# Kernel optimization log

Hardware: AMD Instinct MI355X
Metric: run time of the kernel (lower is better)

## Reference

```python
import jax, jax.numpy as jnp
import numpy as np

V = 32000   # vocab
E = 512     # hidden_size (d_model)
NH = 8      # num_heads
DH = E // NH
NL = 2      # num_layers
FF = 2048   # TransformerDecoderLayer default dim_feedforward
MAXLEN = 24 # cfg.max_length -> gen_len (no target given)
S, B = 48, 8
TRANS = 14
INIT = TRANS - 2            # tgt = transform[1:-1]
LF = INIT + MAXLEN - 1      # final tgt length after the loop
EPS = 1e-5
NEG = -1e9


def pos_encoding(length, d):
    pos = np.arange(length, dtype=np.float32)[:, None]
    div = np.exp(-np.log(10000.0) * np.arange(0, d, 2, dtype=np.float32) / d)
    pe = np.zeros((length, d), dtype=np.float32)
    pe[:, 0::2] = np.sin(pos * div)
    pe[:, 1::2] = np.cos(pos * div)
    return jnp.asarray(pe)


def setup_inputs() -> dict:
    key = jax.random.key(0)
    ks = jax.random.split(key, 12)
    s = 0.02
    return {
        "enc_outputs": jax.random.normal(ks[0], (S, B, E), jnp.float32),
        "transform": jax.random.randint(ks[1], (TRANS, B), 0, V),
        "tf_ratio": 0,
        "emb_table": jax.random.normal(ks[2], (V, E), jnp.float32) * s,
        "sa_w": jax.random.normal(ks[3], (NL, 3 * E, E), jnp.float32) * s,
        "sa_b": jnp.zeros((NL, 3 * E), jnp.float32),
        "sa_ow": jax.random.normal(ks[4], (NL, E, E), jnp.float32) * s,
        "sa_ob": jnp.zeros((NL, E), jnp.float32),
        "ca_w": jax.random.normal(ks[5], (NL, 3 * E, E), jnp.float32) * s,
        "ca_b": jnp.zeros((NL, 3 * E), jnp.float32),
        "ca_ow": jax.random.normal(ks[6], (NL, E, E), jnp.float32) * s,
        "ca_ob": jnp.zeros((NL, E), jnp.float32),
        "ff1_w": jax.random.normal(ks[7], (NL, FF, E), jnp.float32) * s,
        "ff1_b": jnp.zeros((NL, FF), jnp.float32),
        "ff2_w": jax.random.normal(ks[8], (NL, E, FF), jnp.float32) * s,
        "ff2_b": jnp.zeros((NL, E), jnp.float32),
        "ln_g": jnp.ones((NL, 3, E), jnp.float32),
        "ln_b": jnp.zeros((NL, 3, E), jnp.float32),
        "out_w": jax.random.normal(ks[9], (V, E), jnp.float32) * s,
        "out_b": jnp.zeros((V,), jnp.float32),
    }


def _ln(x, g, b):
    m = jnp.mean(x, -1, keepdims=True)
    v = jnp.mean((x - m) ** 2, -1, keepdims=True)
    return (x - m) * jax.lax.rsqrt(v + EPS) * g + b


def _mha(q_in, kv_in, w, b, ow, ob, mask):
    # q_in [Lq,B,E], kv_in [Lk,B,E]; PyTorch packed in_proj [3E,E]
    wq, wk, wv = jnp.split(w, 3, 0)
    bq, bk, bv = jnp.split(b, 3, 0)
    proj = lambda x, wm, bm: (x @ wm.T + bm).reshape(x.shape[0], x.shape[1], NH, DH)
    q, k, v = proj(q_in, wq, bq), proj(kv_in, wk, bk), proj(kv_in, wv, bv)
    sc = jnp.einsum('qbhd,kbhd->bhqk', q, k) / np.sqrt(DH).astype(np.float32)
    if mask is not None:
        sc = sc + mask
    a = jax.nn.softmax(sc, -1)
    o = jnp.einsum('bhqk,kbhd->qbhd', a, v).reshape(q_in.shape[0], q_in.shape[1], E)
    return o @ ow.T + ob


def _decoder(x, mem, mask, p):
    # post-norm TransformerDecoderLayer: self-attn -> cross-attn -> relu FFN
    for l in range(NL):
        x = _ln(x + _mha(x, x, p['sa_w'][l], p['sa_b'][l], p['sa_ow'][l], p['sa_ob'][l], mask),
                p['ln_g'][l, 0], p['ln_b'][l, 0])
        x = _ln(x + _mha(x, mem, p['ca_w'][l], p['ca_b'][l], p['ca_ow'][l], p['ca_ob'][l], None),
                p['ln_g'][l, 1], p['ln_b'][l, 1])
        h = jax.nn.relu(x @ p['ff1_w'][l].T + p['ff1_b'][l]) @ p['ff2_w'][l].T + p['ff2_b'][l]
        x = _ln(x + h, p['ln_g'][l, 2], p['ln_b'][l, 2])
    return x


def reference(enc_outputs, transform, tf_ratio, emb_table, sa_w, sa_b, sa_ow, sa_ob,
              ca_w, ca_b, ca_ow, ca_ob, ff1_w, ff1_b, ff2_w, ff2_b, ln_g, ln_b,
              out_w, out_b):
    # tf_ratio == 0 -> no teacher forcing; gen_len = max_length (no target attr)
    p = dict(sa_w=sa_w, sa_b=sa_b, sa_ow=sa_ow, sa_ob=sa_ob, ca_w=ca_w, ca_b=ca_b,
             ca_ow=ca_ow, ca_ob=ca_ob, ff1_w=ff1_w, ff1_b=ff1_b, ff2_w=ff2_w,
             ff2_b=ff2_b, ln_g=ln_g, ln_b=ln_b)
    pe = pos_encoding(MAXLEN, E)
    # causal mask over the fixed-size buffer; padded (future) slots cannot
    # influence valid positions, so full-buffer passes == torch prefix passes.
    mask = jnp.where(jnp.tril(jnp.ones((LF, LF), bool)), 0.0, NEG)
    tgt0 = emb_table[transform[1:-1]] + pe[:INIT][:, None, :]   # [INIT,B,E]
    buf = jnp.zeros((LF, B, E), jnp.float32).at[:INIT].set(tgt0)

    def step(buf, i):
        h = _decoder(buf, enc_outputs, mask, p)
        pos = INIT - 1 + i                        # last valid position
        pred = jnp.argmax(h[pos] @ out_w.T + out_b, axis=-1)   # [B]
        # torch re-embeds the single predicted token -> PE position 0
        emb = emb_table[pred] + pe[0]
        return buf.at[pos + 1].set(emb), None

    buf, _ = jax.lax.scan(step, buf, jnp.arange(MAXLEN - 1))
    h = _decoder(buf, enc_outputs, mask, p)       # final loop iteration's pass
    return h @ out_w.T + out_b                    # dec_outputs [LF,B,V]
```

## Files before the change

### kernel.cpp

```cpp
#include <hip/hip_runtime.h>
#include <hip/hip_bf16.h>
#include <math.h>

#define V    32000
#define E    512
#define NH   8
#define DH   64
#define NL   2
#define FF   2048
#define MAXLEN 24
#define S    48
#define B    8
#define TRANS 14
#define INIT 12
#define LF   35

#define NB   256
#define NT   512

typedef float f4 __attribute__((ext_vector_type(4)));

__device__ inline float wsum(float v) {
#pragma unroll
  for (int off = 32; off; off >>= 1) v += __shfl_xor(v, off);
  return v;
}
__device__ inline float wmax(float v) {
#pragma unroll
  for (int off = 32; off; off >>= 1) v = fmaxf(v, __shfl_xor(v, off));
  return v;
}

__device__ inline float ldc(const float* p) {
  return __hip_atomic_load(p, __ATOMIC_RELAXED, __HIP_MEMORY_SCOPE_AGENT);
}
__device__ inline void stc(float* p, float v) {
  __hip_atomic_store(p, v, __ATOMIC_RELAXED, __HIP_MEMORY_SCOPE_AGENT);
}
__device__ inline float2 ldc8(const float* p) {
  union { unsigned long long u; float2 f; } c;
  c.u = __hip_atomic_load((const unsigned long long*)p, __ATOMIC_RELAXED, __HIP_MEMORY_SCOPE_AGENT);
  return c.f;
}
__device__ inline void stc8(float* p, float x, float y) {
  union { unsigned long long u; float f[2]; } c; c.f[0] = x; c.f[1] = y;
  __hip_atomic_store((unsigned long long*)p, c.u, __ATOMIC_RELAXED, __HIP_MEMORY_SCOPE_AGENT);
}
__device__ inline int ldci(const int* p) {
  return __hip_atomic_load(p, __ATOMIC_RELAXED, __HIP_MEMORY_SCOPE_AGENT);
}

__device__ inline void ld8_bypass(const float* p, f4* w) {
  asm volatile(
      "global_load_dwordx4 %0, %8, off sc0 sc1 nt\n\t"
      "global_load_dwordx4 %1, %8, off offset:16 sc0 sc1 nt\n\t"
      "global_load_dwordx4 %2, %8, off offset:32 sc0 sc1 nt\n\t"
      "global_load_dwordx4 %3, %8, off offset:48 sc0 sc1 nt\n\t"
      "global_load_dwordx4 %4, %8, off offset:64 sc0 sc1 nt\n\t"
      "global_load_dwordx4 %5, %8, off offset:80 sc0 sc1 nt\n\t"
      "global_load_dwordx4 %6, %8, off offset:96 sc0 sc1 nt\n\t"
      "global_load_dwordx4 %7, %8, off offset:112 sc0 sc1 nt\n\t"
      "s_waitcnt vmcnt(0)"
      : "=&v"(w[0]), "=&v"(w[1]), "=&v"(w[2]), "=&v"(w[3]),
        "=&v"(w[4]), "=&v"(w[5]), "=&v"(w[6]), "=&v"(w[7])
      : "v"(p));
}

#define CMB(v, idx, ov, oi) do { if ((ov) > (v) || ((ov) == (v) && (oi) < (idx))) { (v) = (ov); (idx) = (oi); } } while (0)


__global__ void embed_init_k(const int* __restrict__ transform, const float* __restrict__ emb,
                             float* __restrict__ xbuf) {
  int t = blockIdx.x;
  int pos = t >> 3, b = t & 7;
  int tok = transform[(1 + pos) * B + b];
  for (int d = threadIdx.x; d < E; d += blockDim.x) {
    double div = exp(-log(10000.0) * (double)(d & ~1) / (double)E);
    double ang = (double)pos * div;
    float pe = (d & 1) ? (float)cos(ang) : (float)sin(ang);
    xbuf[(size_t)t * E + d] = emb[(size_t)tok * E + d] + pe;
  }
}

template <int K>
__global__ __launch_bounds__(256) void gemm_k(
    const float* __restrict__ x, const float* __restrict__ W, const float* __restrict__ bias,
    int ntok, int nout, int route, int relu,
    float* __restrict__ out0, float* __restrict__ out1, float* __restrict__ out2) {
  constexpr int K4 = K / 4;
  constexpr int J  = K / 256;
  __shared__ float4 xt[8][K4];
  const int tid = threadIdx.x;
  const int lane = tid & 63;
  const int o = blockIdx.x * 4 + (tid >> 6);

  float4 wr[J];
  if (o < nout) {
    const float4* Wr = (const float4*)(W + (size_t)o * K);
#pragma unroll
    for (int j = 0; j < J; ++j) wr[j] = Wr[lane + 64 * j];
  }

  const int ng = ntok >> 3;
  for (int g = 0; g < ng; ++g) {
    if (g) __syncthreads();
    const float4* xg = (const float4*)(x + (size_t)g * 8 * K);
    float4* xf = &xt[0][0];
    for (int i = tid; i < 8 * K4; i += 256) xf[i] = xg[i];
    __syncthreads();
    if (o < nout) {
      float acc[8] = {0, 0, 0, 0, 0, 0, 0, 0};
#pragma unroll
      for (int j = 0; j < J; ++j) {
        float4 w = wr[j];
#pragma unroll
        for (int tt = 0; tt < 8; ++tt) {
          float4 xv = xt[tt][lane + 64 * j];
          acc[tt] += w.x * xv.x + w.y * xv.y + w.z * xv.z + w.w * xv.w;
        }
      }
#pragma unroll
      for (int tt = 0; tt < 8; ++tt) acc[tt] = wsum(acc[tt]);
      if (lane == 0) {
        float bo = bias[o];
#pragma unroll
        for (int tt = 0; tt < 8; ++tt) {
          float v = acc[tt] + bo;
          if (relu) v = fmaxf(v, 0.f);
          int t = g * 8 + tt;
          if (route == 0) {
            out0[(size_t)t * nout + o] = v;
          } else if (route == 1) {
            if (o < E) out0[(size_t)t * E + o] = v;
            else if (o < 2 * E) out1[(size_t)t * E + (o - E)] = v;
            else out2[(size_t)t * E + (o - 2 * E)] = v;
          } else {
            if (o < E) out0[(size_t)t * E + o] = v;
            else out1[(size_t)t * E + (o - E)] = v;
          }
        }
      }
    }
  }
}

__global__ __launch_bounds__(256) void attn_k(
    const float* __restrict__ q, const float* __restrict__ Kc, const float* __restrict__ Vc,
    float* __restrict__ outp, int p0, int nq, int nk_fixed, int causal) {
  const int tid = threadIdx.x;
  const int lane = tid & 63;
  const int u = blockIdx.x * 4 + (tid >> 6);
  if (u >= nq * 64) return;
  const int qi = u >> 6;
  const int r = u & 63;
  const int b = r >> 3, h = r & 7;
  const int nk = causal ? (p0 + qi + 1) : nk_fixed;

  const size_t qoff = (size_t)(qi * B + b) * E + h * DH + lane;
  const float qv = q[qoff];

  float myscore = -INFINITY;
  for (int k = 0; k < nk; ++k) {
    float prod = qv * Kc[(size_t)(k * B + b) * E + h * DH + lane];
    prod = wsum(prod);
    if (lane == k) myscore = prod * 0.125f;
  }
  float m = wmax(myscore);
  float p = (lane < nk) ? expf(myscore - m) : 0.f;
  float denom = wsum(p);
  float a = p / denom;

  float oacc = 0.f;
  for (int k = 0; k < nk; ++k) {
    float ak = __shfl(a, k);
    oacc = fmaf(ak, Vc[(size_t)(k * B + b) * E + h * DH + lane], oacc);
  }
  outp[qoff] = oacc;
}

__global__ __launch_bounds__(256) void add_ln_k(
    const float* __restrict__ xa, const float* __restrict__ xb,
    const float* __restrict__ g, const float* __restrict__ beta,
    float* __restrict__ outp, int ntok) {
  const int tid = threadIdx.x, lane = tid & 63;
  const int t = blockIdx.x * 4 + (tid >> 6);
  if (t >= ntok) return;
  float v[8];
  float s = 0.f;
#pragma unroll
  for (int j = 0; j < 8; ++j) {
    int d = lane + 64 * j;
    v[j] = xa[(size_t)t * E + d] + xb[(size_t)t * E + d];
    s += v[j];
  }
  s = wsum(s);
  float mean = s * (1.f / 512.f);
  float d2 = 0.f;
#pragma unroll
  for (int j = 0; j < 8; ++j) { float dd = v[j] - mean; d2 += dd * dd; }
  d2 = wsum(d2);
  float inv = 1.f / sqrtf(d2 * (1.f / 512.f) + 1e-5f);
#pragma unroll
  for (int j = 0; j < 8; ++j) {
    int d = lane + 64 * j;
    outp[(size_t)t * E + d] = (v[j] - mean) * inv * g[d] + beta[d];
  }
}

#define B_QKV 0
#define B_OW  6144
#define B_CQ  8192
#define B_COW 10240
#define B_FF1 12288
#define B_FF2 20480
#define SW_TOT 28672

__global__ __launch_bounds__(NT, 1) void decode_persist_k(
    const float* __restrict__ emb,
    const float* __restrict__ sa_w, const float* __restrict__ sa_b,
    const float* __restrict__ sa_ow, const float* __restrict__ sa_ob,
    const float* __restrict__ ca_w, const float* __restrict__ ca_b,
    const float* __restrict__ ca_ow, const float* __restrict__ ca_ob,
    const float* __restrict__ ff1_w, const float* __restrict__ ff1_b,
    const float* __restrict__ ff2_w, const float* __restrict__ ff2_b,
    const float* __restrict__ ln_g, const float* __restrict__ ln_b,
    const float* __restrict__ out_w, const float* __restrict__ out_b,
    float* __restrict__ kself, float* __restrict__ vself,
    const float* __restrict__ kcross, const float* __restrict__ vcross,
    float* __restrict__ xstep, float* __restrict__ qbuf, float* __restrict__ attbuf,
    float* __restrict__ rawbuf, float* __restrict__ x1buf, float* __restrict__ x2buf,
    float* __restrict__ x3buf, float* __restrict__ ybuf, float* __restrict__ hbuf,
    float* __restrict__ pbuf, float* __restrict__ amaxbuf,
    float* __restrict__ outp, int* __restrict__ bar) {
  __shared__ __align__(16) float s_w[SW_TOT];
  __shared__ __align__(16) float s_x[8 * E];
  __shared__ __align__(16) float s_y[8 * E];
  __shared__ __align__(16) float s_q2[64];
  __shared__ float s_rv[NT];
  __shared__ int   s_ri[NT];
  __shared__ float s_pv[8][8];
  __shared__ int   s_pi[8][8];

  const int tid  = threadIdx.x;
  const int lane = tid & 63;
  const int wv   = tid >> 6;
  const int g4   = lane >> 2;
  const int s4   = lane & 3;
  const int bid  = blockIdx.x;
  int gen = 0;

  auto gbar = [&]() {
    ++gen;
    __syncthreads();
    if (tid == 0)
      __hip_atomic_fetch_add(&bar[(bid & 31) * 32], 1, __ATOMIC_RELAXED, __HIP_MEMORY_SCOPE_AGENT);
    if (wv == 0) {
      const int target = gen * 8;
      for (;;) {
        int c = ldci(&bar[(lane & 31) * 32]);
        if (__all(c >= target)) break;
        __builtin_amdgcn_s_sleep(2);
      }
    }
    __syncthreads();
  };

  auto stage_in = [&](float* dst, const float* src) {
    for (int k = tid; k < 2048; k += NT) {
      float2 vv = ldc8(src + 2 * k);
      dst[2 * k] = vv.x; dst[2 * k + 1] = vv.y;
    }
  };
  auto lnstage = [&](int lnidx) {
    const float* gg = ln_g + (size_t)lnidx * E;
    const float* be = ln_b + (size_t)lnidx * E;
    float v[8]; float sum = 0.f;
#pragma unroll
    for (int j = 0; j < 8; ++j) {
      int d = lane + 64 * j;
      v[j] = s_x[wv * E + d] + s_y[wv * E + d];
      sum += v[j];
    }
    sum = wsum(sum);
    float mean = sum * (1.f / 512.f);
    float d2 = 0.f;
#pragma unroll
    for (int j = 0; j < 8; ++j) { float dd = v[j] - mean; d2 += dd * dd; }
    d2 = wsum(d2);
    float inv = 1.f / sqrtf(d2 * (1.f / 512.f) + 1e-5f);
#pragma unroll
    for (int j = 0; j < 8; ++j) {
      int d = lane + 64 * j;
      s_x[wv * E + d] = (v[j] - mean) * inv * gg[d] + be[d];
    }
    __syncthreads();
  };
  auto publish = [&](float* dst) {
    for (int k = tid; k < 256; k += NT)
      stc8(&dst[bid * E + 2 * k], s_x[bid * E + 2 * k], s_x[bid * E + 2 * k + 1]);
  };
  auto proj2 = [&](int wbase, const float* biasp, float* dst) {
    const int row = wv & 1;
    const int r = bid * 2 + row;
    const f4* wp = (const f4*)&s_w[wbase + row * 512];
    f4 w0 = wp[lane], w1 = wp[lane + 64];
    float bias = biasp[r];
#pragma unroll
    for (int half = 0; half < 2; ++half) {
      int b = (wv >> 1) + half * 4;
      const f4* x4 = (const f4*)&s_x[b * E];
      f4 a = w0 * x4[lane] + w1 * x4[lane + 64];
      float acc = a.x + a.y + a.z + a.w;
      acc = wsum(acc);
      if (lane == 0) stc(&dst[b * E + r], acc + bias);
    }
  };
  auto attn_stage = [&](const float* Kbase, const float* Vbase, int nk) {
    const int b = bid >> 3, h = bid & 7;
    if (wv == 0) {
      s_q2[lane] = ldc(&qbuf[b * E + h * DH + lane]);
      float sc = -INFINITY;
      if (lane < nk) {
        const f4* Kr = (const f4*)(Kbase + ((size_t)lane * B + b) * E + h * DH);
        const f4* Qp = (const f4*)s_q2;
        float a0 = 0.f;
#pragma unroll
        for (int u = 0; u < 16; ++u) {
          f4 kv = Kr[u], qv = Qp[u];
          a0 += kv.x * qv.x + kv.y * qv.y + kv.z * qv.z + kv.w * qv.w;
        }
        sc = a0 * 0.125f;
      }
      float m = wmax(sc);
      float e = (lane < nk) ? expf(sc - m) : 0.f;
      float den = wsum(e);
      float aa = e / den;
      float oa = 0.f;
#pragma unroll 4
      for (int k2 = 0; k2 < nk; ++k2) {
        float ak = __shfl(aa, k2);
        oa = fmaf(ak, Vbase[((size_t)k2 * B + b) * E + h * DH + lane], oa);
      }
      stc(&attbuf[b * E + h * DH + lane], oa);
    }
  };

  {
    auto cprow = [&](const float* src, int dstf) {
      f4* d = (f4*)&s_w[dstf];
      const f4* s = (const f4*)src;
      for (int k = tid; k < 128; k += NT) d[k] = s[k];
    };
    const int kc = bid >> 6;
    for (int l = 0; l < NL; ++l) {
      for (int j = 0; j < 6; ++j)
        cprow(sa_w + ((size_t)l * 1536 + bid * 6 + j) * E, B_QKV + (l * 6 + j) * 512);
      for (int j = 0; j < 2; ++j) {
        cprow(sa_ow + ((size_t)l * 512 + bid * 2 + j) * E, B_OW + (l * 2 + j) * 512);
        cprow(ca_w + ((size_t)l * 1536 + bid * 2 + j) * E, B_CQ + (l * 2 + j) * 512);
        cprow(ca_ow + ((size_t)l * 512 + bid * 2 + j) * E, B_COW + (l * 2 + j) * 512);
      }
      for (int j = 0; j < 8; ++j) {
        cprow(ff1_w + ((size_t)l * FF + bid * 8 + j) * E, B_FF1 + (l * 8 + j) * 512);
        cprow(ff2_w + ((size_t)l * 512 + (bid & 63) * 8 + j) * FF + kc * 512,
              B_FF2 + (l * 8 + j) * 512);
      }
    }
    __syncthreads();
  }

  for (int i = 0; i < MAXLEN - 1; ++i) {
    const int p = INIT + i;

    if (bid < 8) {
      const int b = bid;
      if (i == 0) {
        const float* row = outp + ((size_t)(INIT - 1) * B + b) * V;
        float bv = -INFINITY; int bi = 0x7fffffff;
        for (int j2 = tid; j2 < V / 2; j2 += NT) {
          float2 vv = ldc8(row + 2 * j2);
          CMB(bv, bi, vv.x, 2 * j2);
          CMB(bv, bi, vv.y, 2 * j2 + 1);
        }
        s_rv[tid] = bv; s_ri[tid] = bi;
      } else {
        if (tid < 256) {
          float2 pr = ldc8(&amaxbuf[(size_t)(tid * 8 + b) * 2]);
          s_rv[tid] = pr.x; s_ri[tid] = (int)pr.y;
        } else { s_rv[tid] = -INFINITY; s_ri[tid] = 0x7fffffff; }
      }
      __syncthreads();
      for (int st2 = NT / 2; st2; st2 >>= 1) {
        if (tid < st2) {
          float ov = s_rv[tid + st2]; int oi = s_ri[tid + st2];
          CMB(s_rv[tid], s_ri[tid], ov, oi);
        }
        __syncthreads();
      }
      const int tok = s_ri[0];
      if (tid < 256) {
        int d0 = tid * 2;
        float e0 = emb[(size_t)tok * E + d0];
        float e1 = emb[(size_t)tok * E + d0 + 1] + 1.0f;
        stc8(&xstep[(size_t)b * E + d0], e0, e1);
      }
    }
    gbar();

    for (int l = 0; l < NL; ++l) {
      if (l == 0) {
        stage_in(s_x, xstep);
        __syncthreads();
      } else {
        stage_in(s_x, x2buf); stage_in(s_y, ybuf);
        __syncthreads();
        lnstage(2);
        if (bid < 8) publish(x3buf);
      }
      if (wv < 6) {
        const int r = bid * 6 + wv;
        const int sec = r >> 9, off = r & 511;
        const f4* wp = (const f4*)&s_w[B_QKV + (l * 6 + wv) * 512];
        f4 w0 = wp[lane], w1 = wp[lane + 64];
        float bias = sa_b[(size_t)l * 1536 + r];
#pragma unroll
        for (int b = 0; b < 8; ++b) {
          const f4* x4 = (const f4*)&s_x[b * E];
          f4 a = w0 * x4[lane] + w1 * x4[lane + 64];
          float acc = a.x + a.y + a.z + a.w;
          acc = wsum(acc);
          if (lane == 0) {
            acc += bias;
            if (sec == 0) stc(&qbuf[b * E + off], acc);
            else if (sec == 1) stc(&kself[((size_t)(l * LF + p) * B + b) * E + off], acc);
            else stc(&vself[((size_t)(l * LF + p) * B + b) * E + off], acc);
          }
        }
      }
      gbar();
      if (bid < 64) attn_stage(kself + (size_t)l * LF * B * E, vself + (size_t)l * LF * B * E, p + 1);
      gbar();
      stage_in(s_x, attbuf);
      __syncthreads();
      proj2(B_OW + l * 1024, sa_ob + (size_t)l * 512, rawbuf);
      gbar();
      stage_in(s_x, (l == 0) ? xstep : x3buf); stage_in(s_y, rawbuf);
      __syncthreads();
      lnstage(l * 3 + 0);
      if (bid < 8) publish(x1buf);
      proj2(B_CQ + l * 1024, ca_b + (size_t)l * 1536, qbuf);
      gbar();
      if (bid < 64) attn_stage(kcross + (size_t)l * S * B * E, vcross + (size_t)l * S * B * E, S);
      gbar();
      stage_in(s_x, attbuf);
      __syncthreads();
      proj2(B_COW + l * 1024, ca_ob + (size_t)l * 512, rawbuf);
      gbar();
      stage_in(s_x, x1buf); stage_in(s_y, rawbuf);
      __syncthreads();
      lnstage(l * 3 + 1);
      if (bid < 8) publish(x2buf);
      {
        const int r = bid * 8 + wv;
        const f4* wp = (const f4*)&s_w[B_FF1 + (l * 8 + wv) * 512];
        f4 w0 = wp[lane], w1 = wp[lane + 64];
        float bias = ff1_b[(size_t)l * FF + r];
#pragma unroll
        for (int b = 0; b < 8; ++b) {
          const f4* x4 = (const f4*)&s_x[b * E];
          f4 a = w0 * x4[lane] + w1 * x4[lane + 64];
          float acc = a.x + a.y + a.z + a.w;
          acc = wsum(acc);
          if (lane == 0) stc(&hbuf[b * FF + r], fmaxf(acc + bias, 0.f));
        }
      }
      gbar();
      {
        const int kc = bid >> 6;
        for (int k = tid; k < 2048; k += NT) {
          int b = k >> 8, d2 = (k & 255) * 2;
          float2 vv = ldc8(&hbuf[b * FF + kc * 512 + d2]);
          s_x[b * E + d2] = vv.x; s_x[b * E + d2 + 1] = vv.y;
        }
        __syncthreads();
        const int rowf = (bid & 63) * 8 + wv;
        const f4* wp = (const f4*)&s_w[B_FF2 + (l * 8 + wv) * 512];
        f4 w0 = wp[lane], w1 = wp[lane + 64];
#pragma unroll
        for (int b = 0; b < 8; ++b) {
          const f4* x4 = (const f4*)&s_x[b * E];
          f4 a = w0 * x4[lane] + w1 * x4[lane + 64];
          float acc = a.x + a.y + a.z + a.w;
          acc = wsum(acc);
          if (lane == 0) stc(&pbuf[(size_t)(kc * 512 + rowf) * 8 + b], acc);
        }
      }
      gbar();
      {
        const int row = bid * 2 + (wv & 1);
#pragma unroll
        for (int half = 0; half < 2; ++half) {
          int b = (wv >> 1) + half * 4;
          if (lane == 0) {
            float y = ff2_b[(size_t)l * 512 + row];
#pragma unroll
            for (int kc = 0; kc < 4; ++kc) y += ldc(&pbuf[(size_t)(kc * 512 + row) * 8 + b]);
            stc(&ybuf[b * E + row], y);
          }
        }
      }
      gbar();
    }

    stage_in(s_x, x2buf); stage_in(s_y, ybuf);
    __syncthreads();
    lnstage(5);
    {
      const int idx = wv * 16 + g4;
      const bool valid = idx < 125;
      const int r = bid * 125 + idx;
      float acc[8] = {0, 0, 0, 0, 0, 0, 0, 0};
      if (valid) {
        const float* wrow = out_w + (size_t)r * E + s4 * 128;
#pragma unroll
        for (int seg = 0; seg < 4; ++seg) {
          f4 w8[8];
          ld8_bypass(wrow + seg * 32, w8);
#pragma unroll
          for (int b = 0; b < 8; ++b) {
            const f4* x4 = (const f4*)&s_x[b * E + s4 * 128 + seg * 32];
#pragma unroll
            for (int q = 0; q < 8; ++q) {
              f4 xx = x4[q];
              acc[b] += w8[q].x * xx.x + w8[q].y * xx.y + w8[q].z * xx.z + w8[q].w * xx.w;
            }
          }
        }
#pragma unroll
        for (int b = 0; b < 8; ++b) {
          acc[b] += __shfl_xor(acc[b], 1);
          acc[b] += __shfl_xor(acc[b], 2);
          acc[b] += out_b[r];
        }
        if (s4 == 0) {
#pragma unroll
          for (int b = 0; b < 8; ++b)
            stc(&outp[((size_t)p * B + b) * V + r], acc[b]);
        }
      }
#pragma unroll
      for (int b = 0; b < 8; ++b) {
        float v = valid ? acc[b] : -INFINITY;
        int ix = valid ? r : 0x7fffffff;
#pragma unroll
        for (int off = 1; off < 64; off <<= 1) {
          float ov = __shfl_xor(v, off); int oi = __shfl_xor(ix, off);
          CMB(v, ix, ov, oi);
        }
        if (lane == 0) { s_pv[wv][b] = v; s_pi[wv][b] = ix; }
      }
      __syncthreads();
      if (wv == 0) {
        int b = lane & 7, w2 = lane >> 3;
        float v = s_pv[w2][b]; int ix = s_pi[w2][b];
#pragma unroll
        for (int off = 8; off < 64; off <<= 1) {
          float ov = __shfl_xor(v, off); int oi = __shfl_xor(ix, off);
          CMB(v, ix, ov, oi);
        }
        if (lane < 8) stc8(&amaxbuf[(size_t)(bid * 8 + lane) * 2], v, (float)ix);
      }
    }
    gbar();
  }
}

extern "C" void kernel_launch(void* const* d_in, const int* in_sizes, int n_in,
                              void* d_out, int out_size, void* d_ws, size_t ws_size,
                              hipStream_t stream) {
  const float* enc       = (const float*)d_in[0];
  const int*   transform = (const int*)d_in[1];
  const float* emb       = (const float*)d_in[3];
  const float* sa_w  = (const float*)d_in[4];
  const float* sa_b  = (const float*)d_in[5];
  const float* sa_ow = (const float*)d_in[6];
  const float* sa_ob = (const float*)d_in[7];
  const float* ca_w  = (const float*)d_in[8];
  const float* ca_b  = (const float*)d_in[9];
  const float* ca_ow = (const float*)d_in[10];
  const float* ca_ob = (const float*)d_in[11];
  const float* ff1_w = (const float*)d_in[12];
  const float* ff1_b = (const float*)d_in[13];
  const float* ff2_w = (const float*)d_in[14];
  const float* ff2_b = (const float*)d_in[15];
  const float* ln_g  = (const float*)d_in[16];
  const float* ln_b  = (const float*)d_in[17];
  const float* out_w = (const float*)d_in[18];
  const float* out_b = (const float*)d_in[19];
  float* out = (float*)d_out;

  const size_t SELF_SZ  = (size_t)LF * B * E;
  const size_t CROSS_SZ = (size_t)S * B * E;
  float* ws     = (float*)d_ws;
  float* xbuf   = ws;
  float* kself  = xbuf + (size_t)INIT * B * E;
  float* vself  = kself + NL * SELF_SZ;
  float* kcross = vself + NL * SELF_SZ;
  float* vcross = kcross + NL * CROSS_SZ;
  float* xstep  = vcross + NL * CROSS_SZ;
  float* qbuf   = xstep + 8 * E;
  float* attbuf = qbuf + 8 * E;
  float* rawbuf = attbuf + 8 * E;
  float* x1buf  = rawbuf + 8 * E;
  float* x2buf  = x1buf + 8 * E;
  float* x3buf  = x2buf + 8 * E;
  float* ybuf   = x3buf + 8 * E;
  float* hbuf   = ybuf + 8 * E;
  float* pbuf   = hbuf + 8 * FF;
  float* amaxb  = pbuf + 4 * 512 * 8;
  int*   bar    = (int*)(amaxb + 256 * 8 * 2);
  float* act1   = (float*)(bar + 1024);
  float* act2   = act1 + 96 * E;
  float* act3   = act2 + 96 * E;
  float* ffb    = act3 + 96 * E;

  hipMemsetAsync(bar, 0, 4096, stream);

  embed_init_k<<<INIT * B, 128, 0, stream>>>(transform, emb, xbuf);

  for (int l = 0; l < NL; ++l) {
    gemm_k<E><<<(2 * E) / 4, 256, 0, stream>>>(
        enc, ca_w + ((size_t)l * 3 * E + E) * E, ca_b + (size_t)l * 3 * E + E,
        S * B, 2 * E, 2, 0, kcross + l * CROSS_SZ, vcross + l * CROSS_SZ, nullptr);
  }

  {
    const int p0 = 0, nq = INIT, ntok = nq * B;
    const float* xin = xbuf;
    for (int l = 0; l < NL; ++l) {
      const float* x = (l == 0) ? xin : act1;
      gemm_k<E><<<(3 * E) / 4, 256, 0, stream>>>(
          x, sa_w + (size_t)l * 3 * E * E, sa_b + (size_t)l * 3 * E, ntok, 3 * E, 1, 0,
          act2, kself + l * SELF_SZ, vself + l * SELF_SZ);
      attn_k<<<nq * 16, 256, 0, stream>>>(act2, kself + l * SELF_SZ, vself + l * SELF_SZ,
                                          act3, p0, nq, 0, 1);
      gemm_k<E><<<E / 4, 256, 0, stream>>>(
          act3, sa_ow + (size_t)l * E * E, sa_ob + (size_t)l * E, ntok, E, 0, 0, act2, nullptr, nullptr);
      add_ln_k<<<(ntok + 3) / 4, 256, 0, stream>>>(
          x, act2, ln_g + (size_t)l * 3 * E, ln_b + (size_t)l * 3 * E, act1, ntok);
      gemm_k<E><<<E / 4, 256, 0, stream>>>(
          act1, ca_w + (size_t)l * 3 * E * E, ca_b + (size_t)l * 3 * E, ntok, E, 0, 0, act2, nullptr, nullptr);
      attn_k<<<nq * 16, 256, 0, stream>>>(act2, kcross + l * CROSS_SZ, vcross + l * CROSS_SZ,
                                          act3, p0, nq, S, 0);
      gemm_k<E><<<E / 4, 256, 0, stream>>>(
          act3, ca_ow + (size_t)l * E * E, ca_ob + (size_t)l * E, ntok, E, 0, 0, act2, nullptr, nullptr);
      add_ln_k<<<(ntok + 3) / 4, 256, 0, stream>>>(
          act1, act2, ln_g + (size_t)l * 3 * E + E, ln_b + (size_t)l * 3 * E + E, act1, ntok);
      gemm_k<E><<<FF / 4, 256, 0, stream>>>(
          act1, ff1_w + (size_t)l * FF * E, ff1_b + (size_t)l * FF, ntok, FF, 0, 1, ffb, nullptr, nullptr);
      gemm_k<FF><<<E / 4, 256, 0, stream>>>(
          ffb, ff2_w + (size_t)l * E * FF, ff2_b + (size_t)l * E, ntok, E, 0, 0, act2, nullptr, nullptr);
      add_ln_k<<<(ntok + 3) / 4, 256, 0, stream>>>(
          act1, act2, ln_g + (size_t)l * 3 * E + 2 * E, ln_b + (size_t)l * 3 * E + 2 * E, act1, ntok);
    }
    gemm_k<E><<<V / 4, 256, 0, stream>>>(
        act1, out_w, out_b, ntok, V, 0, 0, out, nullptr, nullptr);
  }

  decode_persist_k<<<NB, NT, 0, stream>>>(
      emb, sa_w, sa_b, sa_ow, sa_ob, ca_w, ca_b, ca_ow, ca_ob,
      ff1_w, ff1_b, ff2_w, ff2_b, ln_g, ln_b, out_w, out_b,
      kself, vself, kcross, vcross,
      xstep, qbuf, attbuf, rawbuf, x1buf, x2buf, x3buf, ybuf, hbuf, pbuf, amaxb,
      out, bar);
}
```

Baseline: 5.523 ms.

## Restructure persistent decode kernel: redundant per-block state, fewer grid barriers, 1024 threads

Doubles the block size of the persistent decode kernel. Every block now keeps its own copy of the residual stream and LayerNorm results in LDS, so the separate publish and stage steps are gone. Each block also computes the argmax and embedding itself, which removes a grid barrier at the start of each step. FF2 is rewritten to cover the full K dimension per block, split across layers by block half, which drops the partial-sum buffer and its extra barrier. The grid barrier changes from atomic counters to per-block flag stores, and the output projection switches from nontemporal asm loads to plain vector loads. In exchange, the same work is repeated across all blocks, and each barrier now polls 256 flags.

```diff
diff --git a/kernel.cpp b/kernel.cpp
--- a/kernel.cpp
+++ b/kernel.cpp
@@ -16,7 +16,7 @@
 #define LF   35
 
 #define NB   256
-#define NT   512
+#define NT   1024
 
 typedef float f4 __attribute__((ext_vector_type(4)));
 
@@ -49,21 +49,8 @@
 __device__ inline int ldci(const int* p) {
   return __hip_atomic_load(p, __ATOMIC_RELAXED, __HIP_MEMORY_SCOPE_AGENT);
 }
-
-__device__ inline void ld8_bypass(const float* p, f4* w) {
-  asm volatile(
-      "global_load_dwordx4 %0, %8, off sc0 sc1 nt\n\t"
-      "global_load_dwordx4 %1, %8, off offset:16 sc0 sc1 nt\n\t"
-      "global_load_dwordx4 %2, %8, off offset:32 sc0 sc1 nt\n\t"
-      "global_load_dwordx4 %3, %8, off offset:48 sc0 sc1 nt\n\t"
-      "global_load_dwordx4 %4, %8, off offset:64 sc0 sc1 nt\n\t"
-      "global_load_dwordx4 %5, %8, off offset:80 sc0 sc1 nt\n\t"
-      "global_load_dwordx4 %6, %8, off offset:96 sc0 sc1 nt\n\t"
-      "global_load_dwordx4 %7, %8, off offset:112 sc0 sc1 nt\n\t"
-      "s_waitcnt vmcnt(0)"
-      : "=&v"(w[0]), "=&v"(w[1]), "=&v"(w[2]), "=&v"(w[3]),
-        "=&v"(w[4]), "=&v"(w[5]), "=&v"(w[6]), "=&v"(w[7])
-      : "v"(p));
+__device__ inline void stci(int* p, int v) {
+  __hip_atomic_store(p, v, __ATOMIC_RELAXED, __HIP_MEMORY_SCOPE_AGENT);
 }
 
 #define CMB(v, idx, ov, oi) do { if ((ov) > (v) || ((ov) == (v) && (oi) < (idx))) { (v) = (ov); (idx) = (oi); } } while (0)
@@ -227,93 +214,85 @@
     const float* __restrict__ out_w, const float* __restrict__ out_b,
     float* __restrict__ kself, float* __restrict__ vself,
     const float* __restrict__ kcross, const float* __restrict__ vcross,
-    float* __restrict__ xstep, float* __restrict__ qbuf, float* __restrict__ attbuf,
-    float* __restrict__ rawbuf, float* __restrict__ x1buf, float* __restrict__ x2buf,
-    float* __restrict__ x3buf, float* __restrict__ ybuf, float* __restrict__ hbuf,
-    float* __restrict__ pbuf, float* __restrict__ amaxbuf,
+    float* __restrict__ qbuf, float* __restrict__ attbuf, float* __restrict__ rawbuf,
+    float* __restrict__ hbuf, float* __restrict__ amaxbuf,
     float* __restrict__ outp, int* __restrict__ bar) {
   __shared__ __align__(16) float s_w[SW_TOT];
   __shared__ __align__(16) float s_x[8 * E];
-  __shared__ __align__(16) float s_y[8 * E];
+  __shared__ __align__(16) float s_raw[8 * E];
   __shared__ __align__(16) float s_q2[64];
-  __shared__ float s_rv[NT];
-  __shared__ int   s_ri[NT];
-  __shared__ float s_pv[8][8];
-  __shared__ int   s_pi[8][8];
+  __shared__ __align__(16) float s_attw[64];
+  __shared__ __align__(16) float s_part[4][64];
+  __shared__ int   s_tok[8];
+  __shared__ float s_pv[16][8];
+  __shared__ int   s_pi[16][8];
 
   const int tid  = threadIdx.x;
   const int lane = tid & 63;
   const int wv   = tid >> 6;
-  const int g4   = lane >> 2;
-  const int s4   = lane & 3;
   const int bid  = blockIdx.x;
   int gen = 0;
 
   auto gbar = [&]() {
     ++gen;
     __syncthreads();
-    if (tid == 0)
-      __hip_atomic_fetch_add(&bar[(bid & 31) * 32], 1, __ATOMIC_RELAXED, __HIP_MEMORY_SCOPE_AGENT);
+    if (tid == 0) stci(&bar[bid * 32], gen);
     if (wv == 0) {
-      const int target = gen * 8;
       for (;;) {
-        int c = ldci(&bar[(lane & 31) * 32]);
-        if (__all(c >= target)) break;
-        __builtin_amdgcn_s_sleep(2);
+        int c0 = ldci(&bar[lane * 32]);
+        int c1 = ldci(&bar[(lane + 64) * 32]);
+        int c2 = ldci(&bar[(lane + 128) * 32]);
+        int c3 = ldci(&bar[(lane + 192) * 32]);
+        if (__all(c0 >= gen && c1 >= gen && c2 >= gen && c3 >= gen)) break;
+        __builtin_amdgcn_s_sleep(1);
       }
     }
     __syncthreads();
   };
 
-  auto stage_in = [&](float* dst, const float* src) {
+  auto stage_raw = [&](const float* src) {
     for (int k = tid; k < 2048; k += NT) {
       float2 vv = ldc8(src + 2 * k);
-      dst[2 * k] = vv.x; dst[2 * k + 1] = vv.y;
-    }
+      s_raw[2 * k] = vv.x; s_raw[2 * k + 1] = vv.y;
+    }
+    __syncthreads();
   };
   auto lnstage = [&](int lnidx) {
-    const float* gg = ln_g + (size_t)lnidx * E;
-    const float* be = ln_b + (size_t)lnidx * E;
-    float v[8]; float sum = 0.f;
-#pragma unroll
-    for (int j = 0; j < 8; ++j) {
-      int d = lane + 64 * j;
-      v[j] = s_x[wv * E + d] + s_y[wv * E + d];
-      sum += v[j];
-    }
-    sum = wsum(sum);
-    float mean = sum * (1.f / 512.f);
-    float d2 = 0.f;
-#pragma unroll
-    for (int j = 0; j < 8; ++j) { float dd = v[j] - mean; d2 += dd * dd; }
-    d2 = wsum(d2);
-    float inv = 1.f / sqrtf(d2 * (1.f / 512.f) + 1e-5f);
-#pragma unroll
-    for (int j = 0; j < 8; ++j) {
-      int d = lane + 64 * j;
-      s_x[wv * E + d] = (v[j] - mean) * inv * gg[d] + be[d];
+    if (wv < 8) {
+      const float* gg = ln_g + (size_t)lnidx * E;
+      const float* be = ln_b + (size_t)lnidx * E;
+      float v[8]; float sum = 0.f;
+#pragma unroll
+      for (int j = 0; j < 8; ++j) {
+        int d = lane + 64 * j;
+        v[j] = s_x[wv * E + d] + s_raw[wv * E + d];
+        sum += v[j];
+      }
+      sum = wsum(sum);
+      float mean = sum * (1.f / 512.f);
+      float d2 = 0.f;
+#pragma unroll
+      for (int j = 0; j < 8; ++j) { float dd = v[j] - mean; d2 += dd * dd; }
+      d2 = wsum(d2);
+      float inv = 1.f / sqrtf(d2 * (1.f / 512.f) + 1e-5f);
+#pragma unroll
+      for (int j = 0; j < 8; ++j) {
+        int d = lane + 64 * j;
+        s_x[wv * E + d] = (v[j] - mean) * inv * gg[d] + be[d];
+      }
     }
     __syncthreads();
   };
-  auto publish = [&](float* dst) {
-    for (int k = tid; k < 256; k += NT)
-      stc8(&dst[bid * E + 2 * k], s_x[bid * E + 2 * k], s_x[bid * E + 2 * k + 1]);
-  };
-  auto proj2 = [&](int wbase, const float* biasp, float* dst) {
-    const int row = wv & 1;
-    const int r = bid * 2 + row;
-    const f4* wp = (const f4*)&s_w[wbase + row * 512];
+  auto proj16 = [&](int wbase, const float* srcLDS, const float* biasp, float* dst) {
+    int j = wv & 1, b = wv >> 1;
+    int r = bid * 2 + j;
+    const f4* wp = (const f4*)&s_w[wbase + j * 512];
     f4 w0 = wp[lane], w1 = wp[lane + 64];
-    float bias = biasp[r];
-#pragma unroll
-    for (int half = 0; half < 2; ++half) {
-      int b = (wv >> 1) + half * 4;
-      const f4* x4 = (const f4*)&s_x[b * E];
-      f4 a = w0 * x4[lane] + w1 * x4[lane + 64];
-      float acc = a.x + a.y + a.z + a.w;
-      acc = wsum(acc);
-      if (lane == 0) stc(&dst[b * E + r], acc + bias);
-    }
+    const f4* x4 = (const f4*)(srcLDS + b * E);
+    f4 a = w0 * x4[lane] + w1 * x4[lane + 64];
+    float acc = a.x + a.y + a.z + a.w;
+    acc = wsum(acc);
+    if (lane == 0) stc(&dst[b * E + r], acc + biasp[r]);
   };
   auto attn_stage = [&](const float* Kbase, const float* Vbase, int nk) {
     const int b = bid >> 3, h = bid & 7;
@@ -326,32 +305,34 @@
         float a0 = 0.f;
 #pragma unroll
         for (int u = 0; u < 16; ++u) {
-          f4 kv = Kr[u], qv = Qp[u];
-          a0 += kv.x * qv.x + kv.y * qv.y + kv.z * qv.z + kv.w * qv.w;
+          f4 kv = Kr[u], qq = Qp[u];
+          a0 += kv.x * qq.x + kv.y * qq.y + kv.z * qq.z + kv.w * qq.w;
         }
         sc = a0 * 0.125f;
       }
       float m = wmax(sc);
       float e = (lane < nk) ? expf(sc - m) : 0.f;
       float den = wsum(e);
-      float aa = e / den;
-      float oa = 0.f;
-#pragma unroll 4
-      for (int k2 = 0; k2 < nk; ++k2) {
-        float ak = __shfl(aa, k2);
-        oa = fmaf(ak, Vbase[((size_t)k2 * B + b) * E + h * DH + lane], oa);
-      }
-      stc(&attbuf[b * E + h * DH + lane], oa);
-    }
+      s_attw[lane] = e / den;
+    }
+    __syncthreads();
+    if (wv < 4) {
+      float o = 0.f;
+      for (int k = wv; k < nk; k += 4)
+        o = fmaf(s_attw[k], Vbase[((size_t)k * B + b) * E + h * DH + lane], o);
+      s_part[wv][lane] = o;
+    }
+    __syncthreads();
+    if (wv == 0)
+      stc(&attbuf[b * E + h * DH + lane],
+          s_part[0][lane] + s_part[1][lane] + s_part[2][lane] + s_part[3][lane]);
   };
 
   {
     auto cprow = [&](const float* src, int dstf) {
-      f4* d = (f4*)&s_w[dstf];
-      const f4* s = (const f4*)src;
+      f4* d = (f4*)&s_w[dstf]; const f4* s = (const f4*)src;
       for (int k = tid; k < 128; k += NT) d[k] = s[k];
     };
-    const int kc = bid >> 6;
     for (int l = 0; l < NL; ++l) {
       for (int j = 0; j < 6; ++j)
         cprow(sa_w + ((size_t)l * 1536 + bid * 6 + j) * E, B_QKV + (l * 6 + j) * 512);
@@ -360,11 +341,14 @@
         cprow(ca_w + ((size_t)l * 1536 + bid * 2 + j) * E, B_CQ + (l * 2 + j) * 512);
         cprow(ca_ow + ((size_t)l * 512 + bid * 2 + j) * E, B_COW + (l * 2 + j) * 512);
       }
-      for (int j = 0; j < 8; ++j) {
+      for (int j = 0; j < 8; ++j)
         cprow(ff1_w + ((size_t)l * FF + bid * 8 + j) * E, B_FF1 + (l * 8 + j) * 512);
-        cprow(ff2_w + ((size_t)l * 512 + (bid & 63) * 8 + j) * FF + kc * 512,
-              B_FF2 + (l * 8 + j) * 512);
-      }
+    }
+    const int lf2 = bid >> 7;
+    for (int j = 0; j < 4; ++j) {
+      f4* d = (f4*)&s_w[B_FF2 + j * 2048];
+      const f4* s = (const f4*)(ff2_w + ((size_t)lf2 * 512 + (bid & 127) * 4 + j) * FF);
+      for (int k = tid; k < 512; k += NT) d[k] = s[k];
     }
     __syncthreads();
   }
@@ -372,59 +356,49 @@
   for (int i = 0; i < MAXLEN - 1; ++i) {
     const int p = INIT + i;
 
-    if (bid < 8) {
-      const int b = bid;
+    {
+      int bw = wv & 7;
+      float v = -INFINITY; int ix = 0x7fffffff;
       if (i == 0) {
-        const float* row = outp + ((size_t)(INIT - 1) * B + b) * V;
-        float bv = -INFINITY; int bi = 0x7fffffff;
-        for (int j2 = tid; j2 < V / 2; j2 += NT) {
-          float2 vv = ldc8(row + 2 * j2);
-          CMB(bv, bi, vv.x, 2 * j2);
-          CMB(bv, bi, vv.y, 2 * j2 + 1);
-        }
-        s_rv[tid] = bv; s_ri[tid] = bi;
+        const float* row = outp + ((size_t)(INIT - 1) * B + bw) * V;
+        for (int jj = lane; jj < V / 2; jj += 64) {
+          float2 t = ldc8(row + 2 * jj);
+          CMB(v, ix, t.x, 2 * jj);
+          CMB(v, ix, t.y, 2 * jj + 1);
+        }
       } else {
-        if (tid < 256) {
-          float2 pr = ldc8(&amaxbuf[(size_t)(tid * 8 + b) * 2]);
-          s_rv[tid] = pr.x; s_ri[tid] = (int)pr.y;
-        } else { s_rv[tid] = -INFINITY; s_ri[tid] = 0x7fffffff; }
-      }
+#pragma unroll
+        for (int t = 0; t < 4; ++t) {
+          int e = lane * 4 + t;
+          float2 pr = ldc8(&amaxbuf[(size_t)(e * 8 + bw) * 2]);
+          CMB(v, ix, pr.x, (int)pr.y);
+        }
+      }
+#pragma unroll
+      for (int off = 1; off < 64; off <<= 1) {
+        float ov = __shfl_xor(v, off); int oi = __shfl_xor(ix, off);
+        CMB(v, ix, ov, oi);
+      }
+      if (lane == 0 && wv < 8) s_tok[bw] = ix;
       __syncthreads();
-      for (int st2 = NT / 2; st2; st2 >>= 1) {
-        if (tid < st2) {
-          float ov = s_rv[tid + st2]; int oi = s_ri[tid + st2];
-          CMB(s_rv[tid], s_ri[tid], ov, oi);
-        }
-        __syncthreads();
-      }
-      const int tok = s_ri[0];
-      if (tid < 256) {
-        int d0 = tid * 2;
-        float e0 = emb[(size_t)tok * E + d0];
-        float e1 = emb[(size_t)tok * E + d0 + 1] + 1.0f;
-        stc8(&xstep[(size_t)b * E + d0], e0, e1);
-      }
-    }
-    gbar();
+      int b = tid >> 7, d0 = (tid & 127) * 4;
+      int tok = s_tok[b];
+      float4 ev = *(const float4*)(emb + (size_t)tok * E + d0);
+      s_x[b * E + d0]     = ev.x;
+      s_x[b * E + d0 + 1] = ev.y + 1.0f;
+      s_x[b * E + d0 + 2] = ev.z;
+      s_x[b * E + d0 + 3] = ev.w + 1.0f;
+      __syncthreads();
+    }
 
     for (int l = 0; l < NL; ++l) {
-      if (l == 0) {
-        stage_in(s_x, xstep);
-        __syncthreads();
-      } else {
-        stage_in(s_x, x2buf); stage_in(s_y, ybuf);
-        __syncthreads();
-        lnstage(2);
-        if (bid < 8) publish(x3buf);
-      }
-      if (wv < 6) {
-        const int r = bid * 6 + wv;
-        const int sec = r >> 9, off = r & 511;
-        const f4* wp = (const f4*)&s_w[B_QKV + (l * 6 + wv) * 512];
+      if (wv < 12) {
+        int j = wv >> 1, bg = (wv & 1) * 4;
+        int r = bid * 6 + j, sec = r >> 9, off = r & 511;
+        const f4* wp = (const f4*)&s_w[B_QKV + (l * 6 + j) * 512];
         f4 w0 = wp[lane], w1 = wp[lane + 64];
         float bias = sa_b[(size_t)l * 1536 + r];
-#pragma unroll
-        for (int b = 0; b < 8; ++b) {
+        for (int b = bg; b < bg + 4; ++b) {
           const f4* x4 = (const f4*)&s_x[b * E];
           f4 a = w0 * x4[lane] + w1 * x4[lane + 64];
           float acc = a.x + a.y + a.z + a.w;
@@ -440,33 +414,27 @@
       gbar();
       if (bid < 64) attn_stage(kself + (size_t)l * LF * B * E, vself + (size_t)l * LF * B * E, p + 1);
       gbar();
-      stage_in(s_x, attbuf);
-      __syncthreads();
-      proj2(B_OW + l * 1024, sa_ob + (size_t)l * 512, rawbuf);
-      gbar();
-      stage_in(s_x, (l == 0) ? xstep : x3buf); stage_in(s_y, rawbuf);
-      __syncthreads();
+      stage_raw(attbuf);
+      proj16(B_OW + l * 1024, s_raw, sa_ob + (size_t)l * E, rawbuf);
+      gbar();
+      stage_raw(rawbuf);
       lnstage(l * 3 + 0);
-      if (bid < 8) publish(x1buf);
-      proj2(B_CQ + l * 1024, ca_b + (size_t)l * 1536, qbuf);
+      proj16(B_CQ + l * 1024, s_x, ca_b + (size_t)l * 3 * E, qbuf);
       gbar();
       if (bid < 64) attn_stage(kcross + (size_t)l * S * B * E, vcross + (size_t)l * S * B * E, S);
       gbar();
-      stage_in(s_x, attbuf);
-      __syncthreads();
-      proj2(B_COW + l * 1024, ca_ob + (size_t)l * 512, rawbuf);
-      gbar();
-      stage_in(s_x, x1buf); stage_in(s_y, rawbuf);
-      __syncthreads();
+      stage_raw(attbuf);
+      proj16(B_COW + l * 1024, s_raw, ca_ob + (size_t)l * E, rawbuf);
+      gbar();
+      stage_raw(rawbuf);
       lnstage(l * 3 + 1);
-      if (bid < 8) publish(x2buf);
       {
-        const int r = bid * 8 + wv;
-        const f4* wp = (const f4*)&s_w[B_FF1 + (l * 8 + wv) * 512];
+        int j = wv >> 1, bg = (wv & 1) * 4;
+        int r = bid * 8 + j;
+        const f4* wp = (const f4*)&s_w[B_FF1 + (l * 8 + j) * 512];
         f4 w0 = wp[lane], w1 = wp[lane + 64];
         float bias = ff1_b[(size_t)l * FF + r];
-#pragma unroll
-        for (int b = 0; b < 8; ++b) {
+        for (int b = bg; b < bg + 4; ++b) {
           const f4* x4 = (const f4*)&s_x[b * E];
           f4 a = w0 * x4[lane] + w1 * x4[lane + 64];
           float acc = a.x + a.y + a.z + a.w;
@@ -475,83 +443,80 @@
         }
       }
       gbar();
-      {
-        const int kc = bid >> 6;
-        for (int k = tid; k < 2048; k += NT) {
-          int b = k >> 8, d2 = (k & 255) * 2;
-          float2 vv = ldc8(&hbuf[b * FF + kc * 512 + d2]);
-          s_x[b * E + d2] = vv.x; s_x[b * E + d2 + 1] = vv.y;
-        }
-        __syncthreads();
-        const int rowf = (bid & 63) * 8 + wv;
-        const f4* wp = (const f4*)&s_w[B_FF2 + (l * 8 + wv) * 512];
-        f4 w0 = wp[lane], w1 = wp[lane + 64];
-#pragma unroll
-        for (int b = 0; b < 8; ++b) {
-          const f4* x4 = (const f4*)&s_x[b * E];
-          f4 a = w0 * x4[lane] + w1 * x4[lane + 64];
-          float acc = a.x + a.y + a.z + a.w;
+      if ((bid >> 7) == l) {
+        int b = wv >> 1, j0 = (wv & 1) * 2;
+        int r0 = (bid & 127) * 4;
+        f4 hv[8];
+#pragma unroll
+        for (int j = 0; j < 8; ++j) {
+          const float* hp = hbuf + b * FF + (j * 64 + lane) * 4;
+          float2 a = ldc8(hp), c = ldc8(hp + 2);
+          hv[j].x = a.x; hv[j].y = a.y; hv[j].z = c.x; hv[j].w = c.y;
+        }
+#pragma unroll
+        for (int jr = 0; jr < 2; ++jr) {
+          int rl = j0 + jr;
+          const f4* wp = (const f4*)&s_w[B_FF2 + rl * 2048];
+          float acc = 0.f;
+#pragma unroll
+          for (int j = 0; j < 8; ++j) {
+            f4 w = wp[j * 64 + lane];
+            acc += w.x * hv[j].x + w.y * hv[j].y + w.z * hv[j].z + w.w * hv[j].w;
+          }
           acc = wsum(acc);
-          if (lane == 0) stc(&pbuf[(size_t)(kc * 512 + rowf) * 8 + b], acc);
-        }
-      }
-      gbar();
-      {
-        const int row = bid * 2 + (wv & 1);
-#pragma unroll
-        for (int half = 0; half < 2; ++half) {
-          int b = (wv >> 1) + half * 4;
-          if (lane == 0) {
-            float y = ff2_b[(size_t)l * 512 + row];
-#pragma unroll
-            for (int kc = 0; kc < 4; ++kc) y += ldc(&pbuf[(size_t)(kc * 512 + row) * 8 + b]);
-            stc(&ybuf[b * E + row], y);
-          }
-        }
-      }
-      gbar();
-    }
-
-    stage_in(s_x, x2buf); stage_in(s_y, ybuf);
-    __syncthreads();
-    lnstage(5);
+          if (lane == 0)
+            stc(&rawbuf[b * E + r0 + rl], acc + ff2_b[(size_t)l * 512 + r0 + rl]);
+        }
+      }
+      gbar();
+      stage_raw(rawbuf);
+      lnstage(l * 3 + 2);
+    }
+
     {
-      const int idx = wv * 16 + g4;
+      const int grp = lane >> 3, sub = lane & 7;
+      const int idx = wv * 8 + grp;
       const bool valid = idx < 125;
       const int r = bid * 125 + idx;
       float acc[8] = {0, 0, 0, 0, 0, 0, 0, 0};
       if (valid) {
-        const float* wrow = out_w + (size_t)r * E + s4 * 128;
-#pragma unroll
-        for (int seg = 0; seg < 4; ++seg) {
+        const f4* wrow = (const f4*)(out_w + (size_t)r * E);
+#pragma unroll
+        for (int half = 0; half < 2; ++half) {
           f4 w8[8];
-          ld8_bypass(wrow + seg * 32, w8);
+#pragma unroll
+          for (int j = 0; j < 8; ++j) w8[j] = wrow[(half * 8 + j) * 8 + sub];
 #pragma unroll
           for (int b = 0; b < 8; ++b) {
-            const f4* x4 = (const f4*)&s_x[b * E + s4 * 128 + seg * 32];
-#pragma unroll
-            for (int q = 0; q < 8; ++q) {
-              f4 xx = x4[q];
-              acc[b] += w8[q].x * xx.x + w8[q].y * xx.y + w8[q].z * xx.z + w8[q].w * xx.w;
+            const f4* x4 = (const f4*)&s_x[b * E];
+            float a = 0.f;
+#pragma unroll
+            for (int j = 0; j < 8; ++j) {
+              f4 xx = x4[(half * 8 + j) * 8 + sub];
+              a += w8[j].x * xx.x + w8[j].y * xx.y + w8[j].z * xx.z + w8[j].w * xx.w;
             }
+            acc[b] += a;
           }
         }
 #pragma unroll
         for (int b = 0; b < 8; ++b) {
           acc[b] += __shfl_xor(acc[b], 1);
           acc[b] += __shfl_xor(acc[b], 2);
-          acc[b] += out_b[r];
-        }
-        if (s4 == 0) {
-#pragma unroll
-          for (int b = 0; b < 8; ++b)
+          acc[b] += __shfl_xor(acc[b], 4);
+        }
+        if (sub == 0) {
+          float bo = out_b[r];
+#pragma unroll
+          for (int b = 0; b < 8; ++b) {
+            acc[b] += bo;
             stc(&outp[((size_t)p * B + b) * V + r], acc[b]);
+          }
         }
       }
 #pragma unroll
       for (int b = 0; b < 8; ++b) {
-        float v = valid ? acc[b] : -INFINITY;
-        int ix = valid ? r : 0x7fffffff;
+        float v = (valid && sub == 0) ? acc[b] : -INFINITY;
+        int ix = (valid && sub == 0) ? r : 0x7fffffff;
 #pragma unroll
         for (int off = 1; off < 64; off <<= 1) {
           float ov = __shfl_xor(v, off); int oi = __shfl_xor(ix, off);
@@ -563,6 +528,8 @@
       if (wv == 0) {
         int b = lane & 7, w2 = lane >> 3;
         float v = s_pv[w2][b]; int ix = s_pi[w2][b];
+        float v2 = s_pv[w2 + 8][b]; int ix2 = s_pi[w2 + 8][b];
+        CMB(v, ix, v2, ix2);
 #pragma unroll
         for (int off = 8; off < 64; off <<= 1) {
           float ov = __shfl_xor(v, off); int oi = __shfl_xor(ix, off);
@@ -607,24 +574,18 @@
   float* vself  = kself + NL * SELF_SZ;
   float* kcross = vself + NL * SELF_SZ;
   float* vcross = kcross + NL * CROSS_SZ;
-  float* xstep  = vcross + NL * CROSS_SZ;
-  float* qbuf   = xstep + 8 * E;
+  float* qbuf   = vcross + NL * CROSS_SZ;
   float* attbuf = qbuf + 8 * E;
   float* rawbuf = attbuf + 8 * E;
-  float* x1buf  = rawbuf + 8 * E;
-  float* x2buf  = x1buf + 8 * E;
-  float* x3buf  = x2buf + 8 * E;
-  float* ybuf   = x3buf + 8 * E;
-  float* hbuf   = ybuf + 8 * E;
-  float* pbuf   = hbuf + 8 * FF;
-  float* amaxb  = pbuf + 4 * 512 * 8;
+  float* hbuf   = rawbuf + 8 * E;
+  float* amaxb  = hbuf + 8 * FF;
   int*   bar    = (int*)(amaxb + 256 * 8 * 2);
-  float* act1   = (float*)(bar + 1024);
+  float* act1   = (float*)(bar + 256 * 32);
   float* act2   = act1 + 96 * E;
   float* act3   = act2 + 96 * E;
   float* ffb    = act3 + 96 * E;
 
-  hipMemsetAsync(bar, 0, 4096, stream);
+  hipMemsetAsync(bar, 0, 256 * 32 * 4, stream);
 
   embed_init_k<<<INIT * B, 128, 0, stream>>>(transform, emb, xbuf);
 
@@ -671,6 +632,5 @@
       emb, sa_w, sa_b, sa_ow, sa_ob, ca_w, ca_b, ca_ow, ca_ob,
       ff1_w, ff1_b, ff2_w, ff2_b, ln_g, ln_b, out_w, out_b,
       kself, vself, kcross, vcross,
-      xstep, qbuf, attbuf, rawbuf, x1buf, x2buf, x3buf, ybuf, hbuf, pbuf, amaxb,
-      out, bar);
-}
+      qbuf, attbuf, rawbuf, hbuf, amaxb, out, bar);
+}
```

Measured after the change: 5.474 ms. About the same (-0.9%).
